# Performance work log

Measured on AMD Instinct MI355X. Metric: run time of the kernel, lower is better.

Reference implementation:

```python
import jax, jax.numpy as jnp
import numpy as np

N_NODES = 100000
N_EDGES = 1600000
N_GRAPHS = 256


def setup_inputs() -> dict:
    key = jax.random.key(0)
    ks = jax.random.split(key, 7)
    x = jax.random.normal(ks[0], (N_NODES, 128), dtype=jnp.float32)
    W1 = jax.random.normal(ks[1], (128, 64), dtype=jnp.float32) * (1.0 / np.sqrt(128))
    W2 = jax.random.normal(ks[2], (64, 64), dtype=jnp.float32) * (1.0 / np.sqrt(64))
    W3 = jax.random.normal(ks[3], (64, 64), dtype=jnp.float32) * (1.0 / np.sqrt(64))
    Wlin = jax.random.normal(ks[4], (64, 16), dtype=jnp.float32) * (1.0 / np.sqrt(64))
    edge_index = jax.random.randint(ks[5], (2, N_EDGES), 0, N_NODES, dtype=jnp.int64)
    batch = jnp.sort(jax.random.randint(ks[6], (N_NODES,), 0, N_GRAPHS, dtype=jnp.int64))
    return {"x": x, "W1": W1, "W2": W2, "W3": W3, "Wlin": Wlin,
            "edge_index": edge_index, "batch": batch}


def _gcn_conv(h, W, src, dst):
    # GCNConv(bias=False, normalize=False): scatter-add of transformed src feats onto dst
    m = h @ W                                   # [N, d_out]
    return jax.ops.segment_sum(m[src], dst, num_segments=N_NODES)


def reference(x, W1, W2, W3, Wlin, edge_index, batch):
    src, dst = edge_index[0], edge_index[1]
    h = jax.nn.relu(_gcn_conv(x, W1, src, dst))
    h = jax.nn.relu(_gcn_conv(h, W2, src, dst))
    h = _gcn_conv(h, W3, src, dst)
    # global mean pool over graphs
    sums = jax.ops.segment_sum(h, batch, num_segments=N_GRAPHS)      # [G, d]
    counts = jax.ops.segment_sum(jnp.ones((N_NODES,), h.dtype), batch,
                                 num_segments=N_GRAPHS)              # [G]
    pooled = sums / jnp.maximum(counts, 1.0)[:, None]
    return pooled @ Wlin                                             # [G, out]
```

## Files before the change

### kernel.cpp

```cpp
#include <hip/hip_runtime.h>
#include <hip/hip_bf16.h>

#define SCAN_CHUNK 1024
#define BIN_CHUNK  4096
#define BSH        8
#define BMSK       255
#define NBMAX      512
#define BCAP       5120
#define GSLOTS     16
#define KNODES     2
#define GS16       16
#define GSPLIT     3
#define GSPAN      2048

typedef __attribute__((ext_vector_type(8))) short short8v;
typedef __attribute__((ext_vector_type(4))) float f32x4;

__device__ __forceinline__ unsigned short f2bf(float f) {
    union { float f; unsigned int i; } c;
    c.f = f;
    unsigned int r = c.i + 0x7FFFu + ((c.i >> 16) & 1u);
    return (unsigned short)(r >> 16);
}
__device__ __forceinline__ float lo2f(unsigned int u) {
    union { unsigned int i; float f; } c; c.i = u << 16; return c.f;
}
__device__ __forceinline__ float hi2f(unsigned int u) {
    union { unsigned int i; float f; } c; c.i = u & 0xFFFF0000u; return c.f;
}
__device__ __forceinline__ unsigned int pack2bf(float lo, float hi) {
    return ((unsigned int)f2bf(hi) << 16) | (unsigned int)f2bf(lo);
}
__device__ __forceinline__ int idx_at(const void* p, long long i, int is64) {
    if (is64) return (int)((const long long*)p)[i];
    return ((const int*)p)[i];
}
__device__ __forceinline__ short8v as_s8(uint4 q) {
    return __builtin_bit_cast(short8v, q);
}

__global__ __launch_bounds__(256) void k_setup(const unsigned int* __restrict__ a, long long aWords,
                                               const unsigned int* __restrict__ b, long long bWords,
                                               int* __restrict__ flags, int* __restrict__ bcur,
                                               float* __restrict__ T, int tN,
                                               const float* __restrict__ W1, const float* __restrict__ W2,
                                               const float* __restrict__ W3, const float* __restrict__ Wlin,
                                               float* __restrict__ Wc,
                                               unsigned short* __restrict__ Wt1hi, unsigned short* __restrict__ Wt1lo,
                                               unsigned short* __restrict__ Wt2hi, unsigned short* __restrict__ Wt2lo,
                                               unsigned short* __restrict__ Wcthi, unsigned short* __restrict__ Wctlo) {
    int t = threadIdx.x;
    if (blockIdx.x == 0) {
        __shared__ int sA, sB;
        if (t == 0) { sA = 1; sB = 1; }
        __syncthreads();
        long long hA = aWords / 2;
        long long pA = 2 * ((long long)t * (hA - 1) / 255) + 1;
        if (a[pA] != 0u) atomicAnd(&sA, 0);
        long long hB = bWords / 2;
        long long pB = 2 * ((long long)t * (hB - 1) / 255) + 1;
        if (b[pB] != 0u) atomicAnd(&sB, 0);
        __syncthreads();
        if (t == 0) { flags[0] = sA; flags[1] = sB; }
    } else if (blockIdx.x == 1) {
        bcur[t] = 0; bcur[t + 256] = 0;
        for (int o = t; o < 64 * 16; o += 256) {
            int k = o >> 4, j = o & 15;
            float acc = 0.f;
#pragma unroll 8
            for (int m = 0; m < 64; ++m) acc += W3[k * 64 + m] * Wlin[m * 16 + j];
            Wc[o] = acc;
            unsigned short h = f2bf(acc);
            Wcthi[j * 64 + k] = h;
            Wctlo[j * 64 + k] = f2bf(acc - lo2f(h));
        }
    } else if (blockIdx.x == 2) {
        int col = t >> 2, ks = (t & 3) * 32;
        for (int k = ks; k < ks + 32; ++k) {
            float v = W1[(size_t)k * 64 + col];
            unsigned short h = f2bf(v);
            Wt1hi[col * 128 + k] = h;
            Wt1lo[col * 128 + k] = f2bf(v - lo2f(h));
        }
    } else if (blockIdx.x == 3) {
        int col = t >> 2, ks = (t & 3) * 16;
        for (int k = ks; k < ks + 16; ++k) {
            float v = W2[(size_t)k * 64 + col];
            unsigned short h = f2bf(v);
            Wt2hi[col * 64 + k] = h;
            Wt2lo[col * 64 + k] = f2bf(v - lo2f(h));
        }
    } else {
        int i = (blockIdx.x - 4) * 256 + t;
        if (i < tN) T[i] = 0.f;
    }
}

__global__ __launch_bounds__(256) void k_bin(const void* __restrict__ ei, int nE,
                                             int* __restrict__ bcur, unsigned int* __restrict__ srcsE,
                                             const int* __restrict__ flags) {
    __shared__ int eS[BIN_CHUNK], eD[BIN_CHUNK];
    __shared__ int cntD[NBMAX], baseD[NBMAX], posD[NBMAX];
    int t = threadIdx.x;
    int is64 = flags[0];
    cntD[t] = 0; posD[t] = 0;
    cntD[t + 256] = 0; posD[t + 256] = 0;
    __syncthreads();
    int cs = blockIdx.x * BIN_CHUNK;
    int ce = min(cs + BIN_CHUNK, nE);
    for (int i = cs + t; i < ce; i += 256) {
        int src = idx_at(ei, i, is64);
        int dst = idx_at(ei, (long long)nE + i, is64);
        eS[i - cs] = src; eD[i - cs] = dst;
        atomicAdd(&cntD[dst >> BSH], 1);
    }
    __syncthreads();
    for (int j = t; j < NBMAX; j += 256)
        if (cntD[j] > 0) baseD[j] = atomicAdd(&bcur[j], cntD[j]);
    __syncthreads();
    for (int i = cs + t; i < ce; i += 256) {
        int src = eS[i - cs], dst = eD[i - cs];
        int kd = dst >> BSH;
        int od = baseD[kd] + atomicAdd(&posD[kd], 1);
        if (od < BCAP)
            srcsE[(size_t)kd * BCAP + od] = (unsigned int)src | ((unsigned int)(dst & BMSK) << 17);
    }
}

__global__ __launch_bounds__(256) void k_fill3(unsigned int* __restrict__ srcsE,
                                               const int* __restrict__ bcur,
                                               int* __restrict__ rowstart, int* __restrict__ rowend,
                                               int N, const void* __restrict__ batch,
                                               const int* __restrict__ flags) {
    __shared__ unsigned int ent[BCAP];
    __shared__ int cnt5[256], off5[256], cur5[256], s2[256];
    __shared__ int grelS[256];
    __shared__ int sgf;
    int k = blockIdx.x;
    int t = threadIdx.x;
    int base = k * BCAP;
    int ck = min(bcur[k], BCAP);
    int is64b = flags[1];
    cnt5[t] = 0;
    if (t == 0) sgf = idx_at(batch, (long long)(k << BSH), is64b);
    __syncthreads();
    for (int i = t; i < ck; i += 256) {
        unsigned int v = srcsE[base + i];
        ent[i] = v;
        atomicAdd(&cnt5[v >> 17], 1);
    }
    __syncthreads();
    int c = cnt5[t];
    s2[t] = c;
    __syncthreads();
    for (int off = 1; off < 256; off <<= 1) {
        int x = (t >= off) ? s2[t - off] : 0;
        __syncthreads();
        s2[t] += x;
        __syncthreads();
    }
    int excl = s2[t] - c;
    off5[t] = excl;
    cur5[t] = excl;
    {
        int node = (k << BSH) + t;
        if (node < N) {
            rowstart[node] = base + excl;
            rowend[node]   = base + excl + c;
            grelS[t] = idx_at(batch, node, is64b) - sgf;
        } else {
            grelS[t] = 0;
        }
    }
    __syncthreads();
    for (int i = t; i < ck; i += 256) {
        unsigned int v = ent[i];
        int d = (int)(v >> 17);
        int pos = atomicAdd(&cur5[d], 1);
        srcsE[base + pos] = (v & 0x1FFFFu) | ((unsigned int)grelS[d] << 17);
    }
}

__global__ __launch_bounds__(256) void k_zero_i(int* __restrict__ p, int n) {
    int i = blockIdx.x * 256 + threadIdx.x;
    if (i < n) p[i] = 0;
}
__global__ __launch_bounds__(256) void k_hist(const void* __restrict__ ei, int nE,
                                              int* __restrict__ cnt, const int* __restrict__ flags) {
    int e = blockIdx.x * 256 + threadIdx.x;
    if (e >= nE) return;
    int is64 = flags[0];
    atomicAdd(&cnt[idx_at(ei, (long long)nE + e, is64)], 1);
}
__global__ __launch_bounds__(256) void k_scan_a(const int* __restrict__ cnt, int N, int* __restrict__ bsum) {
    __shared__ int s[256];
    int b = blockIdx.x, t = threadIdx.x;
    int base = b * SCAN_CHUNK + t * 4;
    int v = 0;
#pragma unroll
    for (int j = 0; j < 4; ++j) if (base + j < N) v += cnt[base + j];
    s[t] = v; __syncthreads();
    for (int off = 128; off >= 1; off >>= 1) {
        if (t < off) s[t] += s[t + off];
        __syncthreads();
    }
    if (t == 0) bsum[b] = s[0];
}
__global__ __launch_bounds__(128) void k_scan_b(const int* __restrict__ bsum, int NB, int* __restrict__ bpre) {
    __shared__ int s[128];
    int t = threadIdx.x;
    int v = (t < NB) ? bsum[t] : 0;
    s[t] = v; __syncthreads();
    for (int off = 1; off < 128; off <<= 1) {
        int x = (t >= off) ? s[t - off] : 0;
        __syncthreads();
        s[t] += x;
        __syncthreads();
    }
    if (t < NB) bpre[t] = s[t] - v;
}
__global__ __launch_bounds__(256) void k_scan_c(const int* __restrict__ cnt, int N,
                                                const int* __restrict__ bpre,
                                                int* __restrict__ rowstart, int* __restrict__ rowend,
                                                int* __restrict__ cursor) {
    __shared__ int s[256];
    int b = blockIdx.x, t = threadIdx.x;
    int base = b * SCAN_CHUNK + t * 4;
    int c0 = (base + 0 < N) ? cnt[base + 0] : 0;
    int c1 = (base + 1 < N) ? cnt[base + 1] : 0;
    int c2 = (base + 2 < N) ? cnt[base + 2] : 0;
    int c3 = (base + 3 < N) ? cnt[base + 3] : 0;
    int p0 = c0, p1 = p0 + c1, p2 = p1 + c2, p3 = p2 + c3;
    s[t] = p3; __syncthreads();
    int tot = p3;
    for (int off = 1; off < 256; off <<= 1) {
        int x = (t >= off) ? s[t - off] : 0;
        __syncthreads();
        s[t] += x;
        __syncthreads();
    }
    int toff = s[t] - tot + bpre[b];
    if (base + 0 < N) { rowstart[base + 0] = toff;      rowend[base + 0] = toff + p0; cursor[base + 0] = toff; }
    if (base + 1 < N) { rowstart[base + 1] = toff + p0; rowend[base + 1] = toff + p1; cursor[base + 1] = toff + p0; }
    if (base + 2 < N) { rowstart[base + 2] = toff + p1; rowend[base + 2] = toff + p2; cursor[base + 2] = toff + p1; }
    if (base + 3 < N) { rowstart[base + 3] = toff + p2; rowend[base + 3] = toff + p3; cursor[base + 3] = toff + p2; }
}
__global__ __launch_bounds__(256) void k_fill(const void* __restrict__ ei, int nE,
                                              int* __restrict__ cursor, int* __restrict__ srcs,
                                              const int* __restrict__ flags) {
    int e = blockIdx.x * 256 + threadIdx.x;
    if (e >= nE) return;
    int is64 = flags[0];
    int src = idx_at(ei, e, is64);
    int dst = idx_at(ei, (long long)nE + e, is64);
    int pos = atomicAdd(&cursor[dst], 1);
    srcs[pos] = src;
}

__global__ __launch_bounds__(256) void k_gemm1m(const float* __restrict__ X,
                                                const unsigned short* __restrict__ Wthi,
                                                const unsigned short* __restrict__ Wtlo,
                                                unsigned short* __restrict__ Mb, int N) {
    __shared__ unsigned short Xhi[64 * 128];
    __shared__ unsigned short Xlo[64 * 128];
    int tid = threadIdx.x;
    int wid = tid >> 6, lane = tid & 63;
    int lrow = lane & 15, lk = lane >> 4;
    int base = blockIdx.x * 64;

    uint4 bhi[4], blo[4];
    {
        int col = wid * 16 + lrow;
        const unsigned short* ph = Wthi + col * 128 + lk * 8;
        const unsigned short* pl = Wtlo + col * 128 + lk * 8;
#pragma unroll
        for (int kc = 0; kc < 4; ++kc) {
            bhi[kc] = *(const uint4*)(ph + kc * 32);
            blo[kc] = *(const uint4*)(pl + kc * 32);
        }
    }

    {
        int r = tid >> 2, seg = tid & 3;
        int row = base + r;
        float v[32];
        if (row < N) {
            const float4* src = (const float4*)(X + (size_t)row * 128 + seg * 32);
#pragma unroll
            for (int u = 0; u < 8; ++u) {
                float4 f = src[u];
                v[4 * u] = f.x; v[4 * u + 1] = f.y; v[4 * u + 2] = f.z; v[4 * u + 3] = f.w;
            }
        } else {
#pragma unroll
            for (int u = 0; u < 32; ++u) v[u] = 0.f;
        }
        int swz = (r & 7) << 4;
#pragma unroll
        for (int u = 0; u < 4; ++u) {
            unsigned short h[8];
            float lo[8];
#pragma unroll
            for (int j = 0; j < 8; ++j) {
                float xv = v[u * 8 + j];
                unsigned short hh = f2bf(xv);
                h[j] = hh;
                lo[j] = xv - lo2f(hh);
            }
            uint4 qh, ql;
            qh.x = ((unsigned)h[1] << 16) | h[0]; qh.y = ((unsigned)h[3] << 16) | h[2];
            qh.z = ((unsigned)h[5] << 16) | h[4]; qh.w = ((unsigned)h[7] << 16) | h[6];
            ql.x = pack2bf(lo[0], lo[1]); ql.y = pack2bf(lo[2], lo[3]);
            ql.z = pack2bf(lo[4], lo[5]); ql.w = pack2bf(lo[6], lo[7]);
            int kb = seg * 64 + u * 16;
            int addr = r * 256 + (kb ^ swz);
            *(uint4*)((char*)Xhi + addr) = qh;
            *(uint4*)((char*)Xlo + addr) = ql;
        }
    }
    __syncthreads();

    int col = wid * 16 + lrow;
#pragma unroll
    for (int rt = 0; rt < 4; ++rt) {
        f32x4 acc = {0.f, 0.f, 0.f, 0.f};
        int row = rt * 16 + lrow;
        int rbase = row * 256;
        int swz = (row & 7) << 4;
#pragma unroll
        for (int kc = 0; kc < 4; ++kc) {
            int kb = kc * 64 + lk * 16;
            uint4 ah = *(const uint4*)((const char*)Xhi + rbase + (kb ^ swz));
            uint4 al = *(const uint4*)((const char*)Xlo + rbase + (kb ^ swz));
            acc = __builtin_amdgcn_mfma_f32_16x16x32_bf16(as_s8(ah), as_s8(bhi[kc]), acc, 0, 0, 0);
            acc = __builtin_amdgcn_mfma_f32_16x16x32_bf16(as_s8(al), as_s8(bhi[kc]), acc, 0, 0, 0);
            acc = __builtin_amdgcn_mfma_f32_16x16x32_bf16(as_s8(ah), as_s8(blo[kc]), acc, 0, 0, 0);
        }
#pragma unroll
        for (int j = 0; j < 4; ++j) {
            int orow = base + rt * 16 + lk * 4 + j;
            if (orow < N) Mb[(size_t)orow * 64 + col] = f2bf(acc[j]);
        }
    }
}

__global__ __launch_bounds__(256) void k_projm(const unsigned short* __restrict__ Rb,
                                               const unsigned short* __restrict__ Wthi,
                                               const unsigned short* __restrict__ Wtlo,
                                               unsigned short* __restrict__ Mout, int N) {
    __shared__ unsigned short Rs[64 * 64];
    int tid = threadIdx.x;
    int wid = tid >> 6, lane = tid & 63;
    int lrow = lane & 15, lk = lane >> 4;
    int base = blockIdx.x * 64;

    uint4 bhi[2], blo[2];
    {
        int col = wid * 16 + lrow;
        const unsigned short* ph = Wthi + col * 64 + lk * 8;
        const unsigned short* pl = Wtlo + col * 64 + lk * 8;
#pragma unroll
        for (int kc = 0; kc < 2; ++kc) {
            bhi[kc] = *(const uint4*)(ph + kc * 32);
            blo[kc] = *(const uint4*)(pl + kc * 32);
        }
    }
    {
        int r = tid >> 2, seg = tid & 3;
        int row = base + r;
        uint4 q0, q1;
        if (row < N) {
            const uint4* src = (const uint4*)(Rb + (size_t)row * 64 + seg * 16);
            q0 = src[0]; q1 = src[1];
        } else {
            q0 = make_uint4(0u, 0u, 0u, 0u); q1 = q0;
        }
        int swz = (r & 7) << 4;
        int kb = seg * 32;
        *(uint4*)((char*)Rs + r * 128 + ((kb) ^ swz)) = q0;
        *(uint4*)((char*)Rs + r * 128 + ((kb + 16) ^ swz)) = q1;
    }
    __syncthreads();

    int col = wid * 16 + lrow;
#pragma unroll
    for (int rt = 0; rt < 4; ++rt) {
        f32x4 acc = {0.f, 0.f, 0.f, 0.f};
        int row = rt * 16 + lrow;
        int rbase = row * 128;
        int swz = (row & 7) << 4;
#pragma unroll
        for (int kc = 0; kc < 2; ++kc) {
            int kb = kc * 64 + lk * 16;
            uint4 a = *(const uint4*)((const char*)Rs + rbase + (kb ^ swz));
            acc = __builtin_amdgcn_mfma_f32_16x16x32_bf16(as_s8(a), as_s8(bhi[kc]), acc, 0, 0, 0);
            acc = __builtin_amdgcn_mfma_f32_16x16x32_bf16(as_s8(a), as_s8(blo[kc]), acc, 0, 0, 0);
        }
#pragma unroll
        for (int j = 0; j < 4; ++j) {
            int orow = base + rt * 16 + lk * 4 + j;
            if (orow < N) Mout[(size_t)orow * 64 + col] = f2bf(acc[j]);
        }
    }
}

#define GACC(P)  { A[0] += lo2f((P).x); A[1] += hi2f((P).x);                  \
                   A[2] += lo2f((P).y); A[3] += hi2f((P).y);                  \
                   A[4] += lo2f((P).z); A[5] += hi2f((P).z);                  \
                   A[6] += lo2f((P).w); A[7] += hi2f((P).w); }
#define GATHER8_CORE(SRCS, MB, S, E, LMASK, L, A, MASK)                       \
    {                                                                         \
        int c_ = (S);                                                         \
        for (; c_ + 16 <= (E); c_ += 16) {                                    \
            int sv0_ = (int)(SRCS)[c_ + (L)];                                 \
            int sv1_ = (int)(SRCS)[c_ + 8 + (L)];                             \
            uint4 p_[16];                                                     \
            _Pragma("unroll")                                                 \
            for (int j_ = 0; j_ < 8; ++j_) {                                  \
                int s0_ = __shfl(sv0_, (LMASK) | j_, 64) & (int)(MASK);       \
                p_[j_] = ((const uint4*)((MB) + (size_t)s0_ * 64))[L];        \
            }                                                                 \
            _Pragma("unroll")                                                 \
            for (int j_ = 0; j_ < 8; ++j_) {                                  \
                int s1_ = __shfl(sv1_, (LMASK) | j_, 64) & (int)(MASK);       \
                p_[8 + j_] = ((const uint4*)((MB) + (size_t)s1_ * 64))[L];    \
            }                                                                 \
            _Pragma("unroll")                                                 \
            for (int j_ = 0; j_ < 16; ++j_) GACC(p_[j_])                      \
        }                                                                     \
        if (c_ < (E)) {                                                       \
            int m_ = (E) - c_;                                     \
            int last_ = (E) - 1;                                              \
            int i0_ = c_ + (L); if (i0_ > last_) i0_ = last_;                 \
            int sv0_ = (int)(SRCS)[i0_];                                      \
            uint4 p_[16];                                                     \
            _Pragma("unroll")                                                 \
            for (int j_ = 0; j_ < 8; ++j_) {                                  \
                int s0_ = __shfl(sv0_, (LMASK) | j_, 64) & (int)(MASK);       \
                p_[j_] = ((const uint4*)((MB) + (size_t)s0_ * 64))[L];        \
            }                                                                 \
            if (m_ > 8) {                                                     \
                int i1_ = c_ + 8 + (L); if (i1_ > last_) i1_ = last_;         \
                int sv1_ = (int)(SRCS)[i1_];                                  \
                _Pragma("unroll")                                             \
                for (int j_ = 0; j_ < 8; ++j_) {                              \
                    int s1_ = __shfl(sv1_, (LMASK) | j_, 64) & (int)(MASK);   \
                    p_[8 + j_] = ((const uint4*)((MB) + (size_t)s1_ * 64))[L];\
                }                                                             \
            }                                                                 \
            _Pragma("unroll")                                                 \
            for (int j_ = 0; j_ < 16; ++j_) {                                 \
                if (j_ < m_) GACC(p_[j_])                                     \
            }                                                                 \
        }                                                                     \
    }

__global__ __launch_bounds__(256, 2) void k_gather8(const unsigned short* __restrict__ Mb,
                                                    const int* __restrict__ rowstart,
                                                    const int* __restrict__ rowend,
                                                    const unsigned int* __restrict__ srcs,
                                                    unsigned short* __restrict__ R, int N,
                                                    unsigned int srcMask) {
    int tid = threadIdx.x;
    int lane = tid & 63;
    int l = lane & 7;
    int lmask = lane & 56;
    int node = blockIdx.x * 32 + (tid >> 3);
    if (node >= N) return;
    int s = rowstart[node], e = rowend[node];
    float A[8] = {0.f, 0.f, 0.f, 0.f, 0.f, 0.f, 0.f, 0.f};
    GATHER8_CORE(srcs, Mb, s, e, lmask, l, A, srcMask)
    uint4 q;
    q.x = pack2bf(fmaxf(A[0], 0.f), fmaxf(A[1], 0.f));
    q.y = pack2bf(fmaxf(A[2], 0.f), fmaxf(A[3], 0.f));
    q.z = pack2bf(fmaxf(A[4], 0.f), fmaxf(A[5], 0.f));
    q.w = pack2bf(fmaxf(A[6], 0.f), fmaxf(A[7], 0.f));
    ((uint4*)(R + (size_t)node * 64))[l] = q;
}

__global__ __launch_bounds__(256, 2) void k_gather_y2m(const unsigned short* __restrict__ Mb,
                                                       const int* __restrict__ rowstart,
                                                       const int* __restrict__ rowend,
                                                       const unsigned int* __restrict__ srcs,
                                                       const unsigned short* __restrict__ Wcthi,
                                                       const unsigned short* __restrict__ Wctlo,
                                                       unsigned short* __restrict__ Y2, int N,
                                                       unsigned int srcMask) {
    __shared__ unsigned short Rs[64 * 64];
    int tid = threadIdx.x;
    int lane = tid & 63;
    int l = lane & 7;
    int lmask = lane & 56;
    int rbase0 = blockIdx.x * 64;
    int node0 = rbase0 + (tid >> 3) * KNODES;
#pragma unroll
    for (int jn = 0; jn < KNODES; ++jn) {
        int node = node0 + jn;
        if (node < N) {
            int s = rowstart[node], e = rowend[node];
            float A[8] = {0.f, 0.f, 0.f, 0.f, 0.f, 0.f, 0.f, 0.f};
            GATHER8_CORE(srcs, Mb, s, e, lmask, l, A, srcMask)
            uint4 q;
            q.x = pack2bf(fmaxf(A[0], 0.f), fmaxf(A[1], 0.f));
            q.y = pack2bf(fmaxf(A[2], 0.f), fmaxf(A[3], 0.f));
            q.z = pack2bf(fmaxf(A[4], 0.f), fmaxf(A[5], 0.f));
            q.w = pack2bf(fmaxf(A[6], 0.f), fmaxf(A[7], 0.f));
            int r = node - rbase0;
            int swz = (r & 7) << 4;
            *(uint4*)((char*)Rs + r * 128 + ((l * 16) ^ swz)) = q;
        }
    }
    __syncthreads();

    int wid = tid >> 6;
    int lrow = lane & 15, lk = lane >> 4;
    uint4 bhi[2], blo[2];
#pragma unroll
    for (int kc = 0; kc < 2; ++kc) {
        bhi[kc] = *(const uint4*)(Wcthi + lrow * 64 + kc * 32 + lk * 8);
        blo[kc] = *(const uint4*)(Wctlo + lrow * 64 + kc * 32 + lk * 8);
    }
    f32x4 acc = {0.f, 0.f, 0.f, 0.f};
    int row = wid * 16 + lrow;
    int rb = row * 128;
    int swz = (row & 7) << 4;
#pragma unroll
    for (int kc = 0; kc < 2; ++kc) {
        int kb = kc * 64 + lk * 16;
        uint4 a = *(const uint4*)((const char*)Rs + rb + (kb ^ swz));
        acc = __builtin_amdgcn_mfma_f32_16x16x32_bf16(as_s8(a), as_s8(bhi[kc]), acc, 0, 0, 0);
        acc = __builtin_amdgcn_mfma_f32_16x16x32_bf16(as_s8(a), as_s8(blo[kc]), acc, 0, 0, 0);
    }
#pragma unroll
    for (int j = 0; j < 4; ++j) {
        int orow = rbase0 + wid * 16 + lk * 4 + j;
        if (orow < N) Y2[(size_t)orow * 16 + lrow] = f2bf(acc[j]);
    }
}

__global__ __launch_bounds__(256) void k_gsum16(const unsigned short* __restrict__ y2,
                                                const unsigned int* __restrict__ srcsE,
                                                const int* __restrict__ bcur,
                                                const void* __restrict__ batch,
                                                float* __restrict__ T16, int N, int G,
                                                const int* __restrict__ flags) {
    __shared__ float sacc[GS16][4][16];
    __shared__ int sgmin;
    int t = threadIdx.x;
    int k = blockIdx.x / GSPLIT;
    int part = blockIdx.x % GSPLIT;
    for (int i = t; i < GS16 * 4 * 16; i += 256) ((float*)sacc)[i] = 0.f;
    if (t == 0) sgmin = idx_at(batch, (long long)min(k << BSH, N - 1), flags[1]);
    __syncthreads();
    int gmin = sgmin;
    int ck = min(bcur[k], BCAP);
    int base = k * BCAP;
    int s0 = part * GSPAN + t * 8;
    int m = min(8, ck - s0);
    int rep = t & 3;

#define FLUSH16(GG)                                                           \
    {                                                                         \
        if ((GG) < GS16) {                                                    \
            float* sp_ = &sacc[GG][rep][0];                                   \
            _Pragma("unroll")                                                 \
            for (int j_ = 0; j_ < 16; ++j_) atomicAdd(&sp_[j_], acc[j_]);     \
        } else {                                                              \
            _Pragma("unroll")                                                 \
            for (int j_ = 0; j_ < 16; ++j_)                                   \
                atomicAdd(&T16[(size_t)(gmin + (GG)) * 16 + j_], acc[j_]);    \
        }                                                                     \
    }

    if (m > 0) {
        uint4 ea = *(const uint4*)(srcsE + base + s0);
        uint4 eb = *(const uint4*)(srcsE + base + s0 + 4);
        unsigned ent[8] = {ea.x, ea.y, ea.z, ea.w, eb.x, eb.y, eb.z, eb.w};
        uint4 qa[8], qb[8];
#pragma unroll
        for (int j = 0; j < 8; ++j) {
            unsigned v = (j < m) ? ent[j] : ent[0];
            const uint4* p = (const uint4*)(y2 + (size_t)(v & 0x1FFFFu) * 16);
            qa[j] = p[0];
            qb[j] = p[1];
        }
        float acc[16];
#pragma unroll
        for (int j = 0; j < 16; ++j) acc[j] = 0.f;
        int curg = (int)(ent[0] >> 17);
#pragma unroll
        for (int j = 0; j < 8; ++j) {
            if (j < m) {
                int g = (int)(ent[j] >> 17);
                if (g != curg) {
                    FLUSH16(curg)
#pragma unroll
                    for (int i2 = 0; i2 < 16; ++i2) acc[i2] = 0.f;
                    curg = g;
                }
                acc[0] += lo2f(qa[j].x); acc[1] += hi2f(qa[j].x);
                acc[2] += lo2f(qa[j].y); acc[3] += hi2f(qa[j].y);
                acc[4] += lo2f(qa[j].z); acc[5] += hi2f(qa[j].z);
                acc[6] += lo2f(qa[j].w); acc[7] += hi2f(qa[j].w);
                acc[8] += lo2f(qb[j].x); acc[9] += hi2f(qb[j].x);
                acc[10] += lo2f(qb[j].y); acc[11] += hi2f(qb[j].y);
                acc[12] += lo2f(qb[j].z); acc[13] += hi2f(qb[j].z);
                acc[14] += lo2f(qb[j].w); acc[15] += hi2f(qb[j].w);
            }
        }
        FLUSH16(curg)
    }
    __syncthreads();
    {
        int slot = t >> 4, j = t & 15;
        float v = sacc[slot][0][j] + sacc[slot][1][j] + sacc[slot][2][j] + sacc[slot][3][j];
        int g = gmin + slot;
        if (v != 0.f && g < G) atomicAdd(&T16[(size_t)g * 16 + j], v);
    }
#undef FLUSH16
}

#define GFLUSH(GG, RR)                                                        \
    {                                                                         \
        int slot_ = (GG) - gmin;                                              \
        if (slot_ >= 0 && slot_ < GSLOTS) {                                   \
            _Pragma("unroll")                                                 \
            for (int i_ = 0; i_ < 8; ++i_)                                    \
                atomicAdd(&sacc[slot_][l * 8 + i_], RR[i_]);                  \
        } else {                                                              \
            _Pragma("unroll")                                                 \
            for (int i_ = 0; i_ < 8; ++i_)                                    \
                atomicAdd(&T[(GG) * 64 + l * 8 + i_], RR[i_]);                \
        }                                                                     \
    }

__global__ __launch_bounds__(256) void k_gsum8(const unsigned short* __restrict__ R,
                                               const int* __restrict__ rowstart,
                                               const int* __restrict__ rowend,
                                               const unsigned int* __restrict__ srcs,
                                               const void* __restrict__ batch,
                                               float* __restrict__ T, int N, int G,
                                               const int* __restrict__ flags) {
    __shared__ float sacc[GSLOTS][64];
    int tid = threadIdx.x;
    for (int t = tid; t < GSLOTS * 64; t += 256) ((float*)sacc)[t] = 0.f;
    int is64 = flags[1];
    int nbase = blockIdx.x * 32 * KNODES;
    int gmin = idx_at(batch, min(nbase, N - 1), is64);
    __syncthreads();

    int lane = tid & 63;
    int l = lane & 7;
    int lmask = lane & 56;
    int node0 = nbase + (tid >> 3) * KNODES;
    float r[8] = {0.f, 0.f, 0.f, 0.f, 0.f, 0.f, 0.f, 0.f};
    int curG = -1;
#pragma unroll
    for (int jn = 0; jn < KNODES; ++jn) {
        int node = node0 + jn;
        if (node >= N) break;
        int s = rowstart[node], e = rowend[node];
        float A[8] = {0.f, 0.f, 0.f, 0.f, 0.f, 0.f, 0.f, 0.f};
        GATHER8_CORE(srcs, R, s, e, lmask, l, A, 0xFFFFFFFFu)
        int g = idx_at(batch, node, is64);
        if (g != curG) {
            if (curG >= 0) GFLUSH(curG, r)
#pragma unroll
            for (int i = 0; i < 8; ++i) r[i] = A[i];
            curG = g;
        } else {
#pragma unroll
            for (int i = 0; i < 8; ++i) r[i] += A[i];
        }
    }
    if (curG >= 0) GFLUSH(curG, r)
    __syncthreads();
    for (int t = tid; t < GSLOTS * 64; t += 256) {
        float v = ((float*)sacc)[t];
        int g = gmin + (t >> 6);
        if (v != 0.f && g < G) atomicAdd(&T[g * 64 + (t & 63)], v);
    }
}

__global__ __launch_bounds__(64) void k_out(const float* __restrict__ T,
                                            const void* __restrict__ batch,
                                            const float* __restrict__ Wc,
                                            float* __restrict__ out, int N,
                                            const int* __restrict__ flags) {
    int g = blockIdx.x;
    int lane = threadIdx.x;
    int is64 = flags[1];

    int lo = 0, hi = N;
    while (lo < hi) { int mid = (lo + hi) >> 1; if (idx_at(batch, mid, is64) < g) lo = mid + 1; else hi = mid; }
    int s = lo;
    lo = s; hi = N;
    while (lo < hi) { int mid = (lo + hi) >> 1; if (idx_at(batch, mid, is64) < g + 1) lo = mid + 1; else hi = mid; }
    float cnt = (float)(lo - s);

    __shared__ float P[64];
    P[lane] = T[g * 64 + lane] / fmaxf(cnt, 1.0f);
    __syncthreads();
    if (lane < 16) {
        float o = 0.f;
#pragma unroll 8
        for (int k = 0; k < 64; ++k) o += P[k] * Wc[k * 16 + lane];
        out[g * 16 + lane] = o;
    }
}

__global__ __launch_bounds__(64) void k_out16(const float* __restrict__ T16,
                                              const void* __restrict__ batch,
                                              float* __restrict__ out, int N,
                                              const int* __restrict__ flags) {
    int g = blockIdx.x;
    int lane = threadIdx.x;
    int is64 = flags[1];

    int lo = 0, hi = N;
    while (lo < hi) { int mid = (lo + hi) >> 1; if (idx_at(batch, mid, is64) < g) lo = mid + 1; else hi = mid; }
    int s = lo;
    lo = s; hi = N;
    while (lo < hi) { int mid = (lo + hi) >> 1; if (idx_at(batch, mid, is64) < g + 1) lo = mid + 1; else hi = mid; }
    float cnt = (float)(lo - s);

    if (lane < 16) out[g * 16 + lane] = T16[(size_t)g * 16 + lane] / fmaxf(cnt, 1.0f);
}

extern "C" void kernel_launch(void* const* d_in, const int* in_sizes, int n_in,
                              void* d_out, int out_size, void* d_ws, size_t ws_size,
                              hipStream_t stream) {
    const float* x    = (const float*)d_in[0];
    const float* W1   = (const float*)d_in[1];
    const float* W2   = (const float*)d_in[2];
    const float* W3   = (const float*)d_in[3];
    const float* Wlin = (const float*)d_in[4];
    const void* ei    = d_in[5];
    const void* batch = d_in[6];

    int N  = in_sizes[0] / 128;
    int nE = in_sizes[5] / 2;
    int G  = out_size / 16;
    int NBUCK = (N + (1 << BSH) - 1) >> BSH;
    int NB = (N + SCAN_CHUNK - 1) / SCAN_CHUNK;
    bool fast = (NBUCK <= NBMAX);

    unsigned short* MbA = (unsigned short*)d_ws;
    unsigned short* MbB = (unsigned short*)(MbA + (size_t)N * 64);
    int* ip       = (int*)(MbB + (size_t)N * 64);
    int* rowstart = ip;          ip += N;
    int* rowend   = ip;          ip += N;
    int* cnt      = ip;          ip += N;
    int* bsum     = ip;          ip += 128;
    int* bpre     = ip;          ip += 128;
    int* flags    = ip;          ip += 4;
    int* bcur     = ip;          ip += NBMAX;
    float* T      = (float*)ip;  ip += (size_t)G * 64;
    float* Wc     = (float*)ip;  ip += 64 * 16;
    unsigned short* Wt1hi = (unsigned short*)ip; ip += 4096;
    unsigned short* Wt1lo = (unsigned short*)ip; ip += 4096;
    unsigned short* Wt2hi = (unsigned short*)ip; ip += 2048;
    unsigned short* Wt2lo = (unsigned short*)ip; ip += 2048;
    unsigned short* Wcthi = (unsigned short*)ip; ip += 512;
    unsigned short* Wctlo = (unsigned short*)ip; ip += 512;
    unsigned short* Y2    = (unsigned short*)ip; ip += (size_t)N * 8;
    unsigned int* srcsE = (unsigned int*)ip;
    ip += fast ? (size_t)NBMAX * BCAP : (size_t)nE;
    size_t need = (size_t)((char*)ip - (char*)d_ws);
    if (ws_size < need) return;

    dim3 blk(256);
    int gT64  = (N + 63) / 64;
    int gG1   = (N + 31) / 32;
    int gG2   = (N + 63) / 64;
    int gBin  = (nE + BIN_CHUNK - 1) / BIN_CHUNK;
    int tN    = fast ? G * 16 : G * 64;
    int gSetup = 4 + (tN + 255) / 256;

    hipLaunchKernelGGL(k_setup, dim3(gSetup), blk, 0, stream,
                       (const unsigned int*)ei, (long long)in_sizes[5],
                       (const unsigned int*)batch, (long long)in_sizes[6],
                       flags, bcur, T, tN, W1, W2, W3, Wlin, Wc,
                       Wt1hi, Wt1lo, Wt2hi, Wt2lo, Wcthi, Wctlo);

    if (fast) {
        hipLaunchKernelGGL(k_bin,   dim3(gBin), blk, 0, stream, ei, nE, bcur, srcsE, flags);
        hipLaunchKernelGGL(k_fill3, dim3(NBUCK), blk, 0, stream, srcsE, bcur, rowstart, rowend, N, batch, flags);
    } else {
        int gN = (N + 255) / 256;
        int gE = (nE + 255) / 256;
        hipLaunchKernelGGL(k_zero_i, dim3(gN), blk, 0, stream, cnt, N);
        hipLaunchKernelGGL(k_hist,   dim3(gE), blk, 0, stream, ei, nE, cnt, flags);
        hipLaunchKernelGGL(k_scan_a, dim3(NB), blk, 0, stream, cnt, N, bsum);
        hipLaunchKernelGGL(k_scan_b, dim3(1), dim3(128), 0, stream, bsum, NB, bpre);
        hipLaunchKernelGGL(k_scan_c, dim3(NB), blk, 0, stream, cnt, N, bpre, rowstart, rowend, cnt);
        hipLaunchKernelGGL(k_fill,   dim3(gE), blk, 0, stream, ei, nE, cnt, (int*)srcsE, flags);
    }

    unsigned int srcMask = fast ? 0x1FFFFu : 0xFFFFFFFFu;

    hipLaunchKernelGGL(k_gemm1m,  dim3(gT64), blk, 0, stream, x, Wt1hi, Wt1lo, MbA, N);
    hipLaunchKernelGGL(k_gather8, dim3(gG1), blk, 0, stream, MbA, rowstart, rowend, srcsE, MbB, N, srcMask);
    hipLaunchKernelGGL(k_projm,   dim3(gT64), blk, 0, stream, MbB, Wt2hi, Wt2lo, MbA, N);

    if (fast) {
        hipLaunchKernelGGL(k_gather_y2m, dim3(gG2), blk, 0, stream, MbA, rowstart, rowend, srcsE,
                           Wcthi, Wctlo, Y2, N, srcMask);
        hipLaunchKernelGGL(k_gsum16, dim3(NBUCK * GSPLIT), blk, 0, stream, Y2, srcsE, bcur, batch, T, N, G, flags);
        hipLaunchKernelGGL(k_out16,  dim3(G), dim3(64), 0, stream, T, batch, (float*)d_out, N, flags);
    } else {
        hipLaunchKernelGGL(k_gather8, dim3(gG1), blk, 0, stream, MbA, rowstart, rowend, srcsE, MbB, N, srcMask);
        hipLaunchKernelGGL(k_gsum8, dim3(gG2), blk, 0, stream, MbB, rowstart, rowend, srcsE, batch, T, N, G, flags);
        hipLaunchKernelGGL(k_out, dim3(G), dim3(64), 0, stream, T, batch, Wc, (float*)d_out, N, flags);
    }
}
```

Before: 271.3 us.

## Fuse layer-2 projection into first gather and shrink gather tiles to 32 nodes

A new kernel, k_gather_pm, gathers neighbor rows for 32 nodes into LDS, applies ReLU, and multiplies by W2 with MFMA in the same block. This replaces the separate k_gather8 and k_projm launches and removes one full write and read of the intermediate node matrix through global memory. k_gather_y2m now processes 32 nodes per block with one node per 8-lane group instead of two, which gives more blocks but leaves half the waves idle during the MFMA stage. The slow path keeps the old kernel sequence.

```diff
diff --git a/kernel.cpp b/kernel.cpp
--- a/kernel.cpp
+++ b/kernel.cpp
@@ -455,6 +455,24 @@
         }                                                                     \
     }
 
+#define GATHER_TO_LDS(MB)                                                     \
+    {                                                                         \
+        int node_ = rbase0 + (tid >> 3);                                      \
+        if (node_ < N) {                                                      \
+            int s_ = rowstart[node_], e_ = rowend[node_];                     \
+            float A[8] = {0.f, 0.f, 0.f, 0.f, 0.f, 0.f, 0.f, 0.f};            \
+            GATHER8_CORE(srcs, MB, s_, e_, lmask, l, A, srcMask)              \
+            uint4 q_;                                                         \
+            q_.x = pack2bf(fmaxf(A[0], 0.f), fmaxf(A[1], 0.f));               \
+            q_.y = pack2bf(fmaxf(A[2], 0.f), fmaxf(A[3], 0.f));               \
+            q_.z = pack2bf(fmaxf(A[4], 0.f), fmaxf(A[5], 0.f));               \
+            q_.w = pack2bf(fmaxf(A[6], 0.f), fmaxf(A[7], 0.f));               \
+            int r_ = tid >> 3;                                                \
+            int swz_ = (r_ & 7) << 4;                                         \
+            *(uint4*)((char*)Rs + r_ * 128 + ((l * 16) ^ swz_)) = q_;         \
+        }                                                                     \
+    }
+
 __global__ __launch_bounds__(256, 2) void k_gather8(const unsigned short* __restrict__ Mb,
                                                     const int* __restrict__ rowstart,
                                                     const int* __restrict__ rowend,
@@ -478,6 +496,55 @@
     ((uint4*)(R + (size_t)node * 64))[l] = q;
 }
 
+__global__ __launch_bounds__(256, 2) void k_gather_pm(const unsigned short* __restrict__ Mb,
+                                                      const int* __restrict__ rowstart,
+                                                      const int* __restrict__ rowend,
+                                                      const unsigned int* __restrict__ srcs,
+                                                      const unsigned short* __restrict__ Wthi,
+                                                      const unsigned short* __restrict__ Wtlo,
+                                                      unsigned short* __restrict__ Mout, int N,
+                                                      unsigned int srcMask) {
+    __shared__ unsigned short Rs[32 * 64];
+    int tid = threadIdx.x;
+    int lane = tid & 63;
+    int l = lane & 7;
+    int lmask = lane & 56;
+    int rbase0 = blockIdx.x * 32;
+    GATHER_TO_LDS(Mb)
+    __syncthreads();
+
+    int wid = tid >> 6;
+    int lrow = lane & 15, lk = lane >> 4;
+    int rt = wid >> 1;
+    int ch = wid & 1;
+    int row = rt * 16 + lrow;
+    int rb = row * 128;
+    int swz = (row & 7) << 4;
+#pragma unroll
+    for (int ct = 0; ct < 2; ++ct) {
+        int col = ch * 32 + ct * 16 + lrow;
+        uint4 bhi[2], blo[2];
+#pragma unroll
+        for (int kc = 0; kc < 2; ++kc) {
+            bhi[kc] = *(const uint4*)(Wthi + col * 64 + kc * 32 + lk * 8);
+            blo[kc] = *(const uint4*)(Wtlo + col * 64 + kc * 32 + lk * 8);
+        }
+        f32x4 acc = {0.f, 0.f, 0.f, 0.f};
+#pragma unroll
+        for (int kc = 0; kc < 2; ++kc) {
+            int kb = kc * 64 + lk * 16;
+            uint4 a = *(const uint4*)((const char*)Rs + rb + (kb ^ swz));
+            acc = __builtin_amdgcn_mfma_f32_16x16x32_bf16(as_s8(a), as_s8(bhi[kc]), acc, 0, 0, 0);
+            acc = __builtin_amdgcn_mfma_f32_16x16x32_bf16(as_s8(a), as_s8(blo[kc]), acc, 0, 0, 0);
+        }
+#pragma unroll
+        for (int j = 0; j < 4; ++j) {
+            int orow = rbase0 + rt * 16 + lk * 4 + j;
+            if (orow < N) Mout[(size_t)orow * 64 + col] = f2bf(acc[j]);
+        }
+    }
+}
+
 __global__ __launch_bounds__(256, 2) void k_gather_y2m(const unsigned short* __restrict__ Mb,
                                                        const int* __restrict__ rowstart,
                                                        const int* __restrict__ rowend,
@@ -486,55 +553,40 @@
                                                        const unsigned short* __restrict__ Wctlo,
                                                        unsigned short* __restrict__ Y2, int N,
                                                        unsigned int srcMask) {
-    __shared__ unsigned short Rs[64 * 64];
+    __shared__ unsigned short Rs[32 * 64];
     int tid = threadIdx.x;
     int lane = tid & 63;
     int l = lane & 7;
     int lmask = lane & 56;
-    int rbase0 = blockIdx.x * 64;
-    int node0 = rbase0 + (tid >> 3) * KNODES;
-#pragma unroll
-    for (int jn = 0; jn < KNODES; ++jn) {
-        int node = node0 + jn;
-        if (node < N) {
-            int s = rowstart[node], e = rowend[node];
-            float A[8] = {0.f, 0.f, 0.f, 0.f, 0.f, 0.f, 0.f, 0.f};
-            GATHER8_CORE(srcs, Mb, s, e, lmask, l, A, srcMask)
-            uint4 q;
-            q.x = pack2bf(fmaxf(A[0], 0.f), fmaxf(A[1], 0.f));
-            q.y = pack2bf(fmaxf(A[2], 0.f), fmaxf(A[3], 0.f));
-            q.z = pack2bf(fmaxf(A[4], 0.f), fmaxf(A[5], 0.f));
-            q.w = pack2bf(fmaxf(A[6], 0.f), fmaxf(A[7], 0.f));
-            int r = node - rbase0;
-            int swz = (r & 7) << 4;
-            *(uint4*)((char*)Rs + r * 128 + ((l * 16) ^ swz)) = q;
-        }
-    }
+    int rbase0 = blockIdx.x * 32;
+    GATHER_TO_LDS(Mb)
     __syncthreads();
 
     int wid = tid >> 6;
-    int lrow = lane & 15, lk = lane >> 4;
-    uint4 bhi[2], blo[2];
-#pragma unroll
-    for (int kc = 0; kc < 2; ++kc) {
-        bhi[kc] = *(const uint4*)(Wcthi + lrow * 64 + kc * 32 + lk * 8);
-        blo[kc] = *(const uint4*)(Wctlo + lrow * 64 + kc * 32 + lk * 8);
-    }
-    f32x4 acc = {0.f, 0.f, 0.f, 0.f};
-    int row = wid * 16 + lrow;
-    int rb = row * 128;
-    int swz = (row & 7) << 4;
-#pragma unroll
-    for (int kc = 0; kc < 2; ++kc) {
-        int kb = kc * 64 + lk * 16;
-        uint4 a = *(const uint4*)((const char*)Rs + rb + (kb ^ swz));
-        acc = __builtin_amdgcn_mfma_f32_16x16x32_bf16(as_s8(a), as_s8(bhi[kc]), acc, 0, 0, 0);
-        acc = __builtin_amdgcn_mfma_f32_16x16x32_bf16(as_s8(a), as_s8(blo[kc]), acc, 0, 0, 0);
-    }
-#pragma unroll
-    for (int j = 0; j < 4; ++j) {
-        int orow = rbase0 + wid * 16 + lk * 4 + j;
-        if (orow < N) Y2[(size_t)orow * 16 + lrow] = f2bf(acc[j]);
+    if (wid < 2) {
+        int lrow = lane & 15, lk = lane >> 4;
+        uint4 bhi[2], blo[2];
+#pragma unroll
+        for (int kc = 0; kc < 2; ++kc) {
+            bhi[kc] = *(const uint4*)(Wcthi + lrow * 64 + kc * 32 + lk * 8);
+            blo[kc] = *(const uint4*)(Wctlo + lrow * 64 + kc * 32 + lk * 8);
+        }
+        f32x4 acc = {0.f, 0.f, 0.f, 0.f};
+        int row = wid * 16 + lrow;
+        int rb = row * 128;
+        int swz = (row & 7) << 4;
+#pragma unroll
+        for (int kc = 0; kc < 2; ++kc) {
+            int kb = kc * 64 + lk * 16;
+            uint4 a = *(const uint4*)((const char*)Rs + rb + (kb ^ swz));
+            acc = __builtin_amdgcn_mfma_f32_16x16x32_bf16(as_s8(a), as_s8(bhi[kc]), acc, 0, 0, 0);
+            acc = __builtin_amdgcn_mfma_f32_16x16x32_bf16(as_s8(a), as_s8(blo[kc]), acc, 0, 0, 0);
+        }
+#pragma unroll
+        for (int j = 0; j < 4; ++j) {
+            int orow = rbase0 + wid * 16 + lk * 4 + j;
+            if (orow < N) Y2[(size_t)orow * 16 + lrow] = f2bf(acc[j]);
+        }
     }
 }
 
@@ -800,16 +852,18 @@
     unsigned int srcMask = fast ? 0x1FFFFu : 0xFFFFFFFFu;
 
     hipLaunchKernelGGL(k_gemm1m,  dim3(gT64), blk, 0, stream, x, Wt1hi, Wt1lo, MbA, N);
-    hipLaunchKernelGGL(k_gather8, dim3(gG1), blk, 0, stream, MbA, rowstart, rowend, srcsE, MbB, N, srcMask);
-    hipLaunchKernelGGL(k_projm,   dim3(gT64), blk, 0, stream, MbB, Wt2hi, Wt2lo, MbA, N);
 
     if (fast) {
-        hipLaunchKernelGGL(k_gather_y2m, dim3(gG2), blk, 0, stream, MbA, rowstart, rowend, srcsE,
+        hipLaunchKernelGGL(k_gather_pm, dim3(gG1), blk, 0, stream, MbA, rowstart, rowend, srcsE,
+                           Wt2hi, Wt2lo, MbB, N, srcMask);
+        hipLaunchKernelGGL(k_gather_y2m, dim3(gG1), blk, 0, stream, MbB, rowstart, rowend, srcsE,
                            Wcthi, Wctlo, Y2, N, srcMask);
         hipLaunchKernelGGL(k_gsum16, dim3(NBUCK * GSPLIT), blk, 0, stream, Y2, srcsE, bcur, batch, T, N, G, flags);
         hipLaunchKernelGGL(k_out16,  dim3(G), dim3(64), 0, stream, T, batch, (float*)d_out, N, flags);
     } else {
         hipLaunchKernelGGL(k_gather8, dim3(gG1), blk, 0, stream, MbA, rowstart, rowend, srcsE, MbB, N, srcMask);
+        hipLaunchKernelGGL(k_projm,   dim3(gT64), blk, 0, stream, MbB, Wt2hi, Wt2lo, MbA, N);
+        hipLaunchKernelGGL(k_gather8, dim3(gG1), blk, 0, stream, MbA, rowstart, rowend, srcsE, MbB, N, srcMask);
         hipLaunchKernelGGL(k_gsum8, dim3(gG2), blk, 0, stream, MbB, rowstart, rowend, srcsE, batch, T, N, G, flags);
         hipLaunchKernelGGL(k_out, dim3(G), dim3(64), 0, stream, T, batch, Wc, (float*)d_out, N, flags);
     }
```

New measurement: 259.0 us, median of 2. -4.5%, faster.
